# Kernel optimization log

Measured on AMD Instinct MI355X. Metric: run time of the kernel, lower is better.

## Reference

```python
import jax, jax.numpy as jnp
import numpy as np
from jax import lax

HID = 768; COND = 1280; LAT = 768; NL = 3; V = 128
TEMP = 1.0; TOP_P = 0.9


def setup_inputs() -> dict:
    key = jax.random.key(0)
    ks = iter(jax.random.split(key, 32))
    s = 0.02
    g = 1.0 / float(np.sqrt(HID))
    rn = lambda k, shape, sc: jax.random.normal(k, shape, jnp.float32) * sc
    z1 = lambda n: jnp.zeros((n,), jnp.float32)
    d = {}
    d['p'] = jax.random.normal(next(ks), (1, COND), jnp.float32)
    d['emb_W'] = rn(next(ks), (V, HID), s).at[0].set(0.0)  # padding_idx=0
    d['Wd'] = rn(next(ks), (HID, LAT + COND), s); d['bd'] = z1(HID)
    d['Wih0'] = rn(next(ks), (3 * HID, HID + COND), g); d['Whh0'] = rn(next(ks), (3 * HID, HID), g)
    d['bih0'] = z1(3 * HID); d['bhh0'] = z1(3 * HID)
    for l in (1, 2):
        d[f'Wih{l}'] = rn(next(ks), (3 * HID, HID), g)
        d[f'Whh{l}'] = rn(next(ks), (3 * HID, HID), g)
        d[f'bih{l}'] = z1(3 * HID); d[f'bhh{l}'] = z1(3 * HID)
    d['Wf1'] = rn(next(ks), (HID, COND), s); d['bf1'] = z1(HID)
    d['Wf2'] = rn(next(ks), (2 * HID, HID), s); d['bf2'] = z1(2 * HID)
    d['Wo'] = rn(next(ks), (HID, HID), s)
    d['num_samples'] = 256; d['max_len'] = 64; d['top_k'] = 40
    return d


def _gru_layer(x, h, Wih, Whh, bih, bhh):
    # torch GRU cell: gate order (r, z, n)
    gx = x @ Wih.T + bih          # [B, 3H]
    gh = h @ Whh.T + bhh          # [B, 3H]
    xr, xz, xn = jnp.split(gx, 3, axis=-1)
    hr, hz, hn = jnp.split(gh, 3, axis=-1)
    r = jax.nn.sigmoid(xr + hr)
    z = jax.nn.sigmoid(xz + hz)
    n = jnp.tanh(xn + r * hn)
    return (1.0 - z) * n + z * h


def reference(p, emb_W, Wd, bd,
              Wih0, Whh0, bih0, bhh0,
              Wih1, Whh1, bih1, bhh1,
              Wih2, Whh2, bih2, bhh2,
              Wf1, bf1, Wf2, bf2, Wo,
              num_samples, max_len, top_k):
    B = num_samples
    k_tot = min(top_k, V)
    pe = jnp.broadcast_to(p, (B, COND))                       # p.repeat(B,1)
    z = jax.random.normal(jax.random.key(42), (B, LAT), jnp.float32)
    h0 = jax.nn.gelu(jnp.concatenate([z, pe], axis=1) @ Wd.T + bd, approximate=False)
    h = jnp.tile(h0[None], (NL, 1, 1))                        # [NL, B, H]
    # FiLM params depend only on pe -> hoist out of the decode loop
    fp = jax.nn.gelu(pe @ Wf1.T + bf1, approximate=False) @ Wf2.T + bf2
    gamma, beta = jnp.split(fp, 2, axis=-1)                   # [B, H] each
    cur0 = jnp.ones((B,), jnp.int32)                          # BOS token = 1
    keys = jax.random.split(jax.random.key(7), max_len)
    rows = jnp.arange(B)[:, None]

    def step(carry, k):
        cur, h = carry
        emb = emb_W[cur]                                      # [B, 768]
        x = jnp.concatenate([emb, pe], axis=-1)               # [B, 2048]
        h0n = _gru_layer(x, h[0], Wih0, Whh0, bih0, bhh0)
        h1n = _gru_layer(h0n, h[1], Wih1, Whh1, bih1, bhh1)
        h2n = _gru_layer(h1n, h[2], Wih2, Whh2, bih2, bhh2)
        hn = jnp.stack([h0n, h1n, h2n])
        filmed = h2n * (1.0 + gamma) + beta                   # DeepFiLM on last output
        logits = (filmed @ Wo.T) @ emb_W.T / TEMP             # tied fc_out
        kth = lax.top_k(logits, k_tot)[0][:, -1:]
        logits = jnp.where(logits < kth, -jnp.inf, logits)
        probs = jax.nn.softmax(logits, axis=-1)
        sidx = jnp.argsort(-probs, axis=-1)
        sp = jnp.take_along_axis(probs, sidx, axis=-1)
        rem = jnp.cumsum(sp, axis=-1) > TOP_P
        rem = jnp.concatenate([jnp.zeros_like(rem[:, :1]), rem[:, :-1]], axis=-1)
        rem_orig = jnp.zeros_like(rem).at[rows, sidx].set(rem)
        probs = jnp.where(rem_orig, 0.0, probs)
        nxt = jax.random.categorical(k, jnp.log(probs), axis=-1).astype(jnp.int32)
        return (nxt, hn), nxt

    (_, _), toks = lax.scan(step, (cur0, h), keys)            # toks: [max_len, B]
    seq = jnp.concatenate([cur0[:, None], toks.T], axis=1)    # [B, max_len+1]
    return seq
```

## Files before the change

kernel.cpp:

```cpp
#include <hip/hip_runtime.h>
#include <hip/hip_bf16.h>
#include <stdint.h>

#define HID 768
#define COND 1280
#define NB 256
#define VOC 128
#define TSTEPS 64
#define KTOP 40
#define G3 2304
#define LH (NB*HID)

__device__ __forceinline__ uint32_t rotl32(uint32_t v, int d) {
  return (v << d) | (v >> (32 - d));
}

__device__ __forceinline__ void threefry(uint32_t k0, uint32_t k1,
                                         uint32_t x0, uint32_t x1,
                                         uint32_t& o0, uint32_t& o1) {
  uint32_t k2 = k0 ^ k1 ^ 0x1BD11BDAu;
  x0 += k0; x1 += k1;
#define TF_R(r) { x0 += x1; x1 = rotl32(x1, r); x1 ^= x0; }
  TF_R(13) TF_R(15) TF_R(26) TF_R(6)
  x0 += k1; x1 += k2 + 1u;
  TF_R(17) TF_R(29) TF_R(16) TF_R(24)
  x0 += k2; x1 += k0 + 2u;
  TF_R(13) TF_R(15) TF_R(26) TF_R(6)
  x0 += k0; x1 += k1 + 3u;
  TF_R(17) TF_R(29) TF_R(16) TF_R(24)
  x0 += k1; x1 += k2 + 4u;
  TF_R(13) TF_R(15) TF_R(26) TF_R(6)
  x0 += k2; x1 += k0 + 5u;
#undef TF_R
  o0 = x0; o1 = x1;
}

__device__ __forceinline__ float bits_to_01(uint32_t b) {
  return __uint_as_float((b >> 9) | 0x3f800000u) - 1.0f;
}

__device__ __forceinline__ float gelu_exact(float x) {
  return x * (erff(x / 0x1.6a09e6p+0f) + 1.0f) * 0.5f;
}

__device__ __forceinline__ float sigmoid_(float x) {
  return 0.5f + 0.5f * tanhf(0.5f * x);
}

__global__ __launch_bounds__(256) void k_init(uint32_t* keys, int* cur, int* seq) {
  int tid = threadIdx.x;
  cur[tid] = 1;
  seq[tid * (TSTEPS + 1)] = 1;
  if (tid < 64) {
    uint32_t o0, o1;
    threefry(0u, 7u, 0u, (uint32_t)tid, o0, o1);
    keys[2 * tid] = o0; keys[2 * tid + 1] = o1;
  }
}

__global__ __launch_bounds__(256) void k_z(float* __restrict__ z) {
  int i = blockIdx.x * 256 + threadIdx.x;
  uint32_t o0, o1;
  threefry(0u, 42u, 0u, (uint32_t)i, o0, o1);
  uint32_t bits = o0 ^ o1;
  const float SQ2 = 0x1.6a09e6p+0f;
  const float NM1 = -0x1.fffffep-1f;
  float f = bits_to_01(bits);
  float u = fmaxf(NM1, f * 2.0f + NM1);
  z[i] = SQ2 * erfinvf(u);
}

__global__ __launch_bounds__(256) void k_pe1(const float* __restrict__ p,
    const float* __restrict__ Wd, const float* __restrict__ Wih0,
    const float* __restrict__ Wf1, const float* __restrict__ bf1,
    float* __restrict__ cd, float* __restrict__ c0, float* __restrict__ t1) {
  int g = blockIdx.x, tid = threadIdx.x;
  const float* row;
  if (g < HID)            row = Wd   + (size_t)g * 2048 + HID;
  else if (g < HID + G3)  row = Wih0 + (size_t)(g - HID) * 2048 + HID;
  else                    row = Wf1  + (size_t)(g - HID - G3) * COND;
  float acc = 0.0f;
  for (int k = tid; k < COND; k += 256) acc += p[k] * row[k];
  __shared__ float red[256];
  red[tid] = acc; __syncthreads();
  for (int s = 128; s > 0; s >>= 1) { if (tid < s) red[tid] += red[tid + s]; __syncthreads(); }
  if (tid == 0) {
    if (g < HID) cd[g] = red[0];
    else if (g < HID + G3) c0[g - HID] = red[0];
    else { int j = g - HID - G3; t1[j] = gelu_exact(red[0] + bf1[j]); }
  }
}

__global__ __launch_bounds__(256) void k_pe2(const float* __restrict__ t1,
    const float* __restrict__ Wf2, const float* __restrict__ bf2,
    float* __restrict__ gamma, float* __restrict__ beta) {
  int j = blockIdx.x, tid = threadIdx.x;
  const float* row = Wf2 + (size_t)j * HID;
  float acc = 0.0f;
  for (int k = tid; k < HID; k += 256) acc += t1[k] * row[k];
  __shared__ float red[256];
  red[tid] = acc; __syncthreads();
  for (int s = 128; s > 0; s >>= 1) { if (tid < s) red[tid] += red[tid + s]; __syncthreads(); }
  if (tid == 0) {
    float v = red[0] + bf2[j];
    if (j < HID) gamma[j] = v; else beta[j - HID] = v;
  }
}

template<bool FILM, int EPI>
__global__ __launch_bounds__(256) void k_gemm(
    const float* __restrict__ A, int lda,
    const float* __restrict__ B, int ldb,
    float* __restrict__ C, int N, int Kp, long partStride,
    const float* __restrict__ ga, const float* __restrict__ be,
    const float* __restrict__ e0, const float* __restrict__ e1,
    float* __restrict__ H1, float* __restrict__ H2) {
  __shared__ __align__(16) float As[32][68];
  __shared__ __align__(16) float Bs[32][68];
  const int tid = threadIdx.x;
  const int tm = tid & 15, tn = tid >> 4;
  const int bm = blockIdx.x * 64, bn = blockIdx.y * 64;
  const int kbase = blockIdx.z * Kp;
  const int lr = tid >> 3;
  const int lk = (tid & 7) * 4;
  float acc[4][4] = {};
  for (int k0 = 0; k0 < Kp; k0 += 32) {
    int gk = kbase + k0 + lk;
    float4 av0 = *(const float4*)(A + (size_t)(bm + lr)      * lda + gk);
    float4 av1 = *(const float4*)(A + (size_t)(bm + lr + 32) * lda + gk);
    float4 bv0 = *(const float4*)(B + (size_t)(bn + lr)      * ldb + gk);
    float4 bv1 = *(const float4*)(B + (size_t)(bn + lr + 32) * ldb + gk);
    if (FILM) {
      float4 g = *(const float4*)(ga + gk);
      float4 bb = *(const float4*)(be + gk);
      av0.x = av0.x * (1.0f + g.x) + bb.x; av0.y = av0.y * (1.0f + g.y) + bb.y;
      av0.z = av0.z * (1.0f + g.z) + bb.z; av0.w = av0.w * (1.0f + g.w) + bb.w;
      av1.x = av1.x * (1.0f + g.x) + bb.x; av1.y = av1.y * (1.0f + g.y) + bb.y;
      av1.z = av1.z * (1.0f + g.z) + bb.z; av1.w = av1.w * (1.0f + g.w) + bb.w;
    }
    __syncthreads();
    As[lk + 0][lr] = av0.x; As[lk + 1][lr] = av0.y; As[lk + 2][lr] = av0.z; As[lk + 3][lr] = av0.w;
    As[lk + 0][lr + 32] = av1.x; As[lk + 1][lr + 32] = av1.y; As[lk + 2][lr + 32] = av1.z; As[lk + 3][lr + 32] = av1.w;
    Bs[lk + 0][lr] = bv0.x; Bs[lk + 1][lr] = bv0.y; Bs[lk + 2][lr] = bv0.z; Bs[lk + 3][lr] = bv0.w;
    Bs[lk + 0][lr + 32] = bv1.x; Bs[lk + 1][lr + 32] = bv1.y; Bs[lk + 2][lr + 32] = bv1.z; Bs[lk + 3][lr + 32] = bv1.w;
    __syncthreads();
#pragma unroll
    for (int kk = 0; kk < 32; kk++) {
      float4 a = *(const float4*)&As[kk][tm * 4];
      float4 b = *(const float4*)&Bs[kk][tn * 4];
      acc[0][0] += a.x * b.x; acc[0][1] += a.x * b.y; acc[0][2] += a.x * b.z; acc[0][3] += a.x * b.w;
      acc[1][0] += a.y * b.x; acc[1][1] += a.y * b.y; acc[1][2] += a.y * b.z; acc[1][3] += a.y * b.w;
      acc[2][0] += a.z * b.x; acc[2][1] += a.z * b.y; acc[2][2] += a.z * b.z; acc[2][3] += a.z * b.w;
      acc[3][0] += a.w * b.x; acc[3][1] += a.w * b.y; acc[3][2] += a.w * b.z; acc[3][3] += a.w * b.w;
    }
  }
  if (EPI == 0) {
    float* Cp = C + (size_t)blockIdx.z * (size_t)partStride;
#pragma unroll
    for (int i = 0; i < 4; i++) {
      float4 v; v.x = acc[i][0]; v.y = acc[i][1]; v.z = acc[i][2]; v.w = acc[i][3];
      *(float4*)(Cp + (size_t)(bm + tm * 4 + i) * N + bn + tn * 4) = v;
    }
  } else {
#pragma unroll
    for (int i = 0; i < 4; i++)
#pragma unroll
      for (int j = 0; j < 4; j++) {
        int row = bm + tm * 4 + i, col = bn + tn * 4 + j;
        float v = gelu_exact(acc[i][j] + e0[col] + e1[col]);
        C [(size_t)row * N + col] = v;
        H1[(size_t)row * N + col] = v;
        H2[(size_t)row * N + col] = v;
      }
  }
}

template<bool L0>
__global__ __launch_bounds__(256) void k_gates(
    const float* __restrict__ gxP, const float* __restrict__ ghP,
    const float* __restrict__ E0, const int* __restrict__ cur,
    const float* __restrict__ c0,
    const float* __restrict__ bih, const float* __restrict__ bhh,
    const float* __restrict__ hin, float* __restrict__ hout) {
  int idx = blockIdx.x * 256 + threadIdx.x;
  int b = idx / HID, j = idx - b * HID;
  const long S = (long)NB * G3;
  long base = (long)b * G3;
  float xr, xz, xn;
  if (L0) {
    const float* e = E0 + (size_t)cur[b] * G3;
    xr = e[j]           + c0[j]           + bih[j];
    xz = e[j + HID]     + c0[j + HID]     + bih[j + HID];
    xn = e[j + 2 * HID] + c0[j + 2 * HID] + bih[j + 2 * HID];
  } else {
    xr = gxP[base + j]           + gxP[S + base + j]           + bih[j];
    xz = gxP[base + j + HID]     + gxP[S + base + j + HID]     + bih[j + HID];
    xn = gxP[base + j + 2 * HID] + gxP[S + base + j + 2 * HID] + bih[j + 2 * HID];
  }
  float hr = ghP[base + j]           + ghP[S + base + j]           + bhh[j];
  float hz = ghP[base + j + HID]     + ghP[S + base + j + HID]     + bhh[j + HID];
  float hn = ghP[base + j + 2 * HID] + ghP[S + base + j + 2 * HID] + bhh[j + 2 * HID];
  float r  = sigmoid_(xr + hr);
  float zg = sigmoid_(xz + hz);
  float n  = tanhf(xn + r * hn);
  float h  = hin[idx];
  hout[idx] = (1.0f - zg) * n + zg * h;
}

__global__ __launch_bounds__(256) void k_sample(
    const float* __restrict__ oP, const float* __restrict__ embW,
    const uint32_t* __restrict__ keys, int t,
    int* __restrict__ cur, int* __restrict__ seq) {
  const int b = blockIdx.x, tid = threadIdx.x;
  __shared__ __align__(16) float o[HID];
  __shared__ float logit[VOC];
  __shared__ float gum[VOC];
  __shared__ float prob[VOC];
  __shared__ float skey[VOC];
  __shared__ int   sidx[VOC];
  __shared__ float rv[VOC];
  __shared__ int   ri[VOC];
  __shared__ float sden;
  const long OS = (long)NB * HID;
  for (int k = tid; k < HID; k += 256) {
    long ix = (long)b * HID + k;
    o[k] = ((oP[ix] + oP[OS + ix]) + oP[2 * OS + ix]) + oP[3 * OS + ix];
  }
  __syncthreads();
  if (tid < VOC) {
    const float4* ew = (const float4*)(embW + (size_t)tid * HID);
    const float4* ov = (const float4*)o;
    float a0 = 0, a1 = 0, a2 = 0, a3 = 0;
#pragma unroll 4
    for (int q = 0; q < HID / 4; q++) {
      float4 w = ew[q]; float4 x = ov[q];
      a0 += w.x * x.x; a1 += w.y * x.y; a2 += w.z * x.z; a3 += w.w * x.w;
    }
    logit[tid] = (a0 + a1) + (a2 + a3);
  } else {
    int v = tid - VOC;
    int i = b * VOC + v;
    uint32_t o0, o1;
    uint32_t kk0 = keys[2 * t], kk1 = keys[2 * t + 1];
    threefry(kk0, kk1, 0u, (uint32_t)i, o0, o1);
    uint32_t bits = o0 ^ o1;
    float f = bits_to_01(bits);
    float u = f + 0x1p-126f;
    u = fmaxf(0x1p-126f, u);
    gum[v] = -logf(-logf(u));
  }
  __syncthreads();
  if (tid < VOC) { skey[tid] = logit[tid]; sidx[tid] = tid; }
  for (int ksz = 2; ksz <= VOC; ksz <<= 1) {
    for (int jsz = ksz >> 1; jsz > 0; jsz >>= 1) {
      __syncthreads();
      if (tid < VOC) {
        int ixj = tid ^ jsz;
        if (ixj > tid) {
          float ka = skey[tid], kb = skey[ixj];
          int ia = sidx[tid], ib = sidx[ixj];
          bool ab = (ka > kb) || (ka == kb && ia < ib);
          bool up = ((tid & ksz) == 0);
          if (up ? !ab : ab) {
            skey[tid] = kb; skey[ixj] = ka; sidx[tid] = ib; sidx[ixj] = ia;
          }
        }
      }
    }
  }
  __syncthreads();
  float m = skey[0], kth = skey[KTOP - 1];
  __syncthreads();
  if (tid < VOC) {
    float l = logit[tid];
    prob[tid] = (l < kth) ? 0.0f : expf(l - m);
  }
  __syncthreads();
  if (tid < VOC) rv[tid] = prob[tid];
  __syncthreads();
  for (int s = 64; s > 0; s >>= 1) { if (tid < s) rv[tid] += rv[tid + s]; __syncthreads(); }
  if (tid == 0) sden = rv[0];
  __syncthreads();
  if (tid < VOC) {
    prob[tid] = prob[tid] / sden;
    skey[tid] = prob[tid];
    sidx[tid] = tid;
  }
  for (int ksz = 2; ksz <= VOC; ksz <<= 1) {
    for (int jsz = ksz >> 1; jsz > 0; jsz >>= 1) {
      __syncthreads();
      if (tid < VOC) {
        int ixj = tid ^ jsz;
        if (ixj > tid) {
          float ka = skey[tid], kb = skey[ixj];
          int ia = sidx[tid], ib = sidx[ixj];
          bool ab = (ka > kb) || (ka == kb && ia < ib);
          bool up = ((tid & ksz) == 0);
          if (up ? !ab : ab) {
            skey[tid] = kb; skey[ixj] = ka; sidx[tid] = ib; sidx[ixj] = ia;
          }
        }
      }
    }
  }
  __syncthreads();
  if (tid == 0) {
    float c = 0.0f;
    for (int i2 = 0; i2 < VOC; i2++) {
      float pv = skey[i2];
      if (i2 > 0 && c > 0.9f) prob[sidx[i2]] = 0.0f;
      c += pv;
    }
  }
  __syncthreads();
  if (tid < VOC) { rv[tid] = logf(prob[tid]) + gum[tid]; ri[tid] = tid; }
  __syncthreads();
  for (int s = 64; s > 0; s >>= 1) {
    if (tid < s) {
      float vb = rv[tid + s]; int ib2 = ri[tid + s];
      if (vb > rv[tid] || (vb == rv[tid] && ib2 < ri[tid])) { rv[tid] = vb; ri[tid] = ib2; }
    }
    __syncthreads();
  }
  if (tid == 0) { int v = ri[0]; cur[b] = v; seq[b * (TSTEPS + 1) + t + 1] = v; }
}

extern "C" void kernel_launch(void* const* d_in, const int* in_sizes, int n_in,
                              void* d_out, int out_size, void* d_ws, size_t ws_size,
                              hipStream_t stream) {
  const float* p    = (const float*)d_in[0];
  const float* embW = (const float*)d_in[1];
  const float* Wd   = (const float*)d_in[2];
  const float* bd   = (const float*)d_in[3];
  const float* Wih0 = (const float*)d_in[4];
  const float* Whh0 = (const float*)d_in[5];
  const float* bih0 = (const float*)d_in[6];
  const float* bhh0 = (const float*)d_in[7];
  const float* Wih1 = (const float*)d_in[8];
  const float* Whh1 = (const float*)d_in[9];
  const float* bih1 = (const float*)d_in[10];
  const float* bhh1 = (const float*)d_in[11];
  const float* Wih2 = (const float*)d_in[12];
  const float* Whh2 = (const float*)d_in[13];
  const float* bih2 = (const float*)d_in[14];
  const float* bhh2 = (const float*)d_in[15];
  const float* Wf1  = (const float*)d_in[16];
  const float* bf1  = (const float*)d_in[17];
  const float* Wf2  = (const float*)d_in[18];
  const float* bf2  = (const float*)d_in[19];
  const float* Wo   = (const float*)d_in[20];
  int* seq = (int*)d_out;

  float* w = (float*)d_ws;
  float* z     = w;
  float* E0    = z + 196608;
  float* cd    = E0 + 294912;
  float* c0    = cd + 768;
  float* t1    = c0 + 2304;
  float* gamma = t1 + 768;
  float* beta  = gamma + 768;
  float* HA    = beta + 768;
  float* HB    = HA + 589824;
  float* gxP   = HB + 589824;
  float* ghP   = gxP + 1179648;
  float* oP    = ghP + 1179648;
  uint32_t* keys = (uint32_t*)(oP + 786432);
  int* cur = (int*)(keys + 128);

  const long PS_G = (long)NB * G3;
  const long PS_O = (long)NB * HID;

  k_init<<<1, 256, 0, stream>>>(keys, cur, seq);
  k_z<<<768, 256, 0, stream>>>(z);
  k_pe1<<<HID + G3 + HID, 256, 0, stream>>>(p, Wd, Wih0, Wf1, bf1, cd, c0, t1);
  k_pe2<<<2 * HID, 256, 0, stream>>>(t1, Wf2, bf2, gamma, beta);
  k_gemm<false, 0><<<dim3(2, 36, 1), 256, 0, stream>>>(embW, HID, Wih0, 2048, E0,
      G3, HID, 0L, nullptr, nullptr, nullptr, nullptr, nullptr, nullptr);
  k_gemm<false, 1><<<dim3(4, 12, 1), 256, 0, stream>>>(z, HID, Wd, 2048, HA,
      HID, HID, 0L, nullptr, nullptr, cd, bd, HA + LH, HA + 2 * LH);

  for (int t = 0; t < TSTEPS; t++) {
    float* Hin  = (t & 1) ? HB : HA;
    float* Hout = (t & 1) ? HA : HB;
    k_gemm<false, 0><<<dim3(4, 36, 2), 256, 0, stream>>>(Hin, HID, Whh0, HID, ghP,
        G3, 384, PS_G, nullptr, nullptr, nullptr, nullptr, nullptr, nullptr);
    k_gates<true><<<768, 256, 0, stream>>>(nullptr, ghP, E0, cur, c0, bih0, bhh0, Hin, Hout);
    k_gemm<false, 0><<<dim3(4, 36, 2), 256, 0, stream>>>(Hout, HID, Wih1, HID, gxP,
        G3, 384, PS_G, nullptr, nullptr, nullptr, nullptr, nullptr, nullptr);
    k_gemm<false, 0><<<dim3(4, 36, 2), 256, 0, stream>>>(Hin + LH, HID, Whh1, HID, ghP,
        G3, 384, PS_G, nullptr, nullptr, nullptr, nullptr, nullptr, nullptr);
    k_gates<false><<<768, 256, 0, stream>>>(gxP, ghP, nullptr, nullptr, nullptr,
        bih1, bhh1, Hin + LH, Hout + LH);
    k_gemm<false, 0><<<dim3(4, 36, 2), 256, 0, stream>>>(Hout + LH, HID, Wih2, HID, gxP,
        G3, 384, PS_G, nullptr, nullptr, nullptr, nullptr, nullptr, nullptr);
    k_gemm<false, 0><<<dim3(4, 36, 2), 256, 0, stream>>>(Hin + 2 * LH, HID, Whh2, HID, ghP,
        G3, 384, PS_G, nullptr, nullptr, nullptr, nullptr, nullptr, nullptr);
    k_gates<false><<<768, 256, 0, stream>>>(gxP, ghP, nullptr, nullptr, nullptr,
        bih2, bhh2, Hin + 2 * LH, Hout + 2 * LH);
    k_gemm<true, 0><<<dim3(4, 12, 4), 256, 0, stream>>>(Hout + 2 * LH, HID, Wo, HID, oP,
        HID, 192, PS_O, gamma, beta, nullptr, nullptr, nullptr, nullptr);
    k_sample<<<256, 256, 0, stream>>>(oP, embW, keys, t, cur, seq);
  }
}
```

Before: 13.21 ms.

## Replace split-K GEMMs with smaller-tile full-K GEMM and batch paired layer GEMMs

Adds a new GEMM kernel with smaller output tiles (64x32 or 32x32) that runs the full K dimension, so the split-K partial buffers and their reduction inside the gate and sampling kernels go away. The input-to-hidden and hidden-to-hidden GEMMs for layers 1 and 2 are merged into one launch via blockIdx.z, which cuts kernel launches per step. The FiLM GEMM uses a 32-row tile with more blocks. In exchange, each block runs a longer K loop with a simpler, lower-reuse register tile (2 columns per thread), which may lower arithmetic intensity.

```diff
diff --git a/kernel.cpp b/kernel.cpp
--- a/kernel.cpp
+++ b/kernel.cpp
@@ -175,16 +175,77 @@
   }
 }
 
+template<int MT, bool FILM>
+__global__ __launch_bounds__(256) void k_gemm2(
+    const float* __restrict__ A0, const float* __restrict__ B0, float* __restrict__ C0,
+    const float* __restrict__ A1, const float* __restrict__ B1, float* __restrict__ C1,
+    int N, int K,
+    const float* __restrict__ ga, const float* __restrict__ be) {
+  const float* A = blockIdx.z ? A1 : A0;
+  const float* B = blockIdx.z ? B1 : B0;
+  float*       C = blockIdx.z ? C1 : C0;
+  __shared__ __align__(16) float As[32][MT + 4];
+  __shared__ __align__(16) float Bs[32][36];
+  const int tid = threadIdx.x;
+  const int bm = blockIdx.x * MT, bn = blockIdx.y * 32;
+  const int lr = tid >> 3;
+  const int lk = (tid & 7) * 4;
+  constexpr int RPT = MT / 16;
+  const int tm = tid & 15, tn = tid >> 4;
+  float acc[RPT][2] = {};
+  for (int k0 = 0; k0 < K; k0 += 32) {
+    float4 av[MT / 32];
+#pragma unroll
+    for (int r = 0; r < MT / 32; r++) {
+      av[r] = *(const float4*)(A + (size_t)(bm + lr + r * 32) * K + k0 + lk);
+      if (FILM) {
+        float4 g  = *(const float4*)(ga + k0 + lk);
+        float4 bb = *(const float4*)(be + k0 + lk);
+        av[r].x = av[r].x * (1.0f + g.x) + bb.x;
+        av[r].y = av[r].y * (1.0f + g.y) + bb.y;
+        av[r].z = av[r].z * (1.0f + g.z) + bb.z;
+        av[r].w = av[r].w * (1.0f + g.w) + bb.w;
+      }
+    }
+    float4 bv = *(const float4*)(B + (size_t)(bn + lr) * K + k0 + lk);
+    __syncthreads();
+#pragma unroll
+    for (int r = 0; r < MT / 32; r++) {
+      As[lk + 0][lr + r * 32] = av[r].x;
+      As[lk + 1][lr + r * 32] = av[r].y;
+      As[lk + 2][lr + r * 32] = av[r].z;
+      As[lk + 3][lr + r * 32] = av[r].w;
+    }
+    Bs[lk + 0][lr] = bv.x; Bs[lk + 1][lr] = bv.y;
+    Bs[lk + 2][lr] = bv.z; Bs[lk + 3][lr] = bv.w;
+    __syncthreads();
+#pragma unroll
+    for (int kk = 0; kk < 32; kk++) {
+      float b0 = Bs[kk][tn * 2], b1 = Bs[kk][tn * 2 + 1];
+#pragma unroll
+      for (int i = 0; i < RPT; i++) {
+        float a = As[kk][tm * RPT + i];
+        acc[i][0] += a * b0;
+        acc[i][1] += a * b1;
+      }
+    }
+  }
+#pragma unroll
+  for (int i = 0; i < RPT; i++) {
+    float2 v; v.x = acc[i][0]; v.y = acc[i][1];
+    *(float2*)(C + (size_t)(bm + tm * RPT + i) * N + bn + tn * 2) = v;
+  }
+}
+
 template<bool L0>
 __global__ __launch_bounds__(256) void k_gates(
-    const float* __restrict__ gxP, const float* __restrict__ ghP,
+    const float* __restrict__ gx, const float* __restrict__ gh,
     const float* __restrict__ E0, const int* __restrict__ cur,
     const float* __restrict__ c0,
     const float* __restrict__ bih, const float* __restrict__ bhh,
     const float* __restrict__ hin, float* __restrict__ hout) {
   int idx = blockIdx.x * 256 + threadIdx.x;
   int b = idx / HID, j = idx - b * HID;
-  const long S = (long)NB * G3;
   long base = (long)b * G3;
   float xr, xz, xn;
   if (L0) {
@@ -193,13 +254,13 @@
     xz = e[j + HID]     + c0[j + HID]     + bih[j + HID];
     xn = e[j + 2 * HID] + c0[j + 2 * HID] + bih[j + 2 * HID];
   } else {
-    xr = gxP[base + j]           + gxP[S + base + j]           + bih[j];
-    xz = gxP[base + j + HID]     + gxP[S + base + j + HID]     + bih[j + HID];
-    xn = gxP[base + j + 2 * HID] + gxP[S + base + j + 2 * HID] + bih[j + 2 * HID];
-  }
-  float hr = ghP[base + j]           + ghP[S + base + j]           + bhh[j];
-  float hz = ghP[base + j + HID]     + ghP[S + base + j + HID]     + bhh[j + HID];
-  float hn = ghP[base + j + 2 * HID] + ghP[S + base + j + 2 * HID] + bhh[j + 2 * HID];
+    xr = gx[base + j]           + bih[j];
+    xz = gx[base + j + HID]     + bih[j + HID];
+    xn = gx[base + j + 2 * HID] + bih[j + 2 * HID];
+  }
+  float hr = gh[base + j]           + bhh[j];
+  float hz = gh[base + j + HID]     + bhh[j + HID];
+  float hn = gh[base + j + 2 * HID] + bhh[j + 2 * HID];
   float r  = sigmoid_(xr + hr);
   float zg = sigmoid_(xz + hz);
   float n  = tanhf(xn + r * hn);
@@ -221,11 +282,7 @@
   __shared__ float rv[VOC];
   __shared__ int   ri[VOC];
   __shared__ float sden;
-  const long OS = (long)NB * HID;
-  for (int k = tid; k < HID; k += 256) {
-    long ix = (long)b * HID + k;
-    o[k] = ((oP[ix] + oP[OS + ix]) + oP[2 * OS + ix]) + oP[3 * OS + ix];
-  }
+  for (int k = tid; k < HID; k += 256) o[k] = oP[(long)b * HID + k];
   __syncthreads();
   if (tid < VOC) {
     const float4* ew = (const float4*)(embW + (size_t)tid * HID);
@@ -361,14 +418,11 @@
   float* beta  = gamma + 768;
   float* HA    = beta + 768;
   float* HB    = HA + 589824;
-  float* gxP   = HB + 589824;
-  float* ghP   = gxP + 1179648;
-  float* oP    = ghP + 1179648;
-  uint32_t* keys = (uint32_t*)(oP + 786432);
+  float* gx    = HB + 589824;
+  float* gh    = gx + 589824;
+  float* oP    = gh + 589824;
+  uint32_t* keys = (uint32_t*)(oP + 196608);
   int* cur = (int*)(keys + 128);
-
-  const long PS_G = (long)NB * G3;
-  const long PS_O = (long)NB * HID;
 
   k_init<<<1, 256, 0, stream>>>(keys, cur, seq);
   k_z<<<768, 256, 0, stream>>>(z);
@@ -382,23 +436,19 @@
   for (int t = 0; t < TSTEPS; t++) {
     float* Hin  = (t & 1) ? HB : HA;
     float* Hout = (t & 1) ? HA : HB;
-    k_gemm<false, 0><<<dim3(4, 36, 2), 256, 0, stream>>>(Hin, HID, Whh0, HID, ghP,
-        G3, 384, PS_G, nullptr, nullptr, nullptr, nullptr, nullptr, nullptr);
-    k_gates<true><<<768, 256, 0, stream>>>(nullptr, ghP, E0, cur, c0, bih0, bhh0, Hin, Hout);
-    k_gemm<false, 0><<<dim3(4, 36, 2), 256, 0, stream>>>(Hout, HID, Wih1, HID, gxP,
-        G3, 384, PS_G, nullptr, nullptr, nullptr, nullptr, nullptr, nullptr);
-    k_gemm<false, 0><<<dim3(4, 36, 2), 256, 0, stream>>>(Hin + LH, HID, Whh1, HID, ghP,
-        G3, 384, PS_G, nullptr, nullptr, nullptr, nullptr, nullptr, nullptr);
-    k_gates<false><<<768, 256, 0, stream>>>(gxP, ghP, nullptr, nullptr, nullptr,
+    k_gemm2<64, false><<<dim3(4, 72, 1), 256, 0, stream>>>(
+        Hin, Whh0, gh, nullptr, nullptr, nullptr, G3, HID, nullptr, nullptr);
+    k_gates<true><<<768, 256, 0, stream>>>(nullptr, gh, E0, cur, c0, bih0, bhh0, Hin, Hout);
+    k_gemm2<64, false><<<dim3(4, 72, 2), 256, 0, stream>>>(
+        Hout, Wih1, gx, Hin + LH, Whh1, gh, G3, HID, nullptr, nullptr);
+    k_gates<false><<<768, 256, 0, stream>>>(gx, gh, nullptr, nullptr, nullptr,
         bih1, bhh1, Hin + LH, Hout + LH);
-    k_gemm<false, 0><<<dim3(4, 36, 2), 256, 0, stream>>>(Hout + LH, HID, Wih2, HID, gxP,
-        G3, 384, PS_G, nullptr, nullptr, nullptr, nullptr, nullptr, nullptr);
-    k_gemm<false, 0><<<dim3(4, 36, 2), 256, 0, stream>>>(Hin + 2 * LH, HID, Whh2, HID, ghP,
-        G3, 384, PS_G, nullptr, nullptr, nullptr, nullptr, nullptr, nullptr);
-    k_gates<false><<<768, 256, 0, stream>>>(gxP, ghP, nullptr, nullptr, nullptr,
+    k_gemm2<64, false><<<dim3(4, 72, 2), 256, 0, stream>>>(
+        Hout + LH, Wih2, gx, Hin + 2 * LH, Whh2, gh, G3, HID, nullptr, nullptr);
+    k_gates<false><<<768, 256, 0, stream>>>(gx, gh, nullptr, nullptr, nullptr,
         bih2, bhh2, Hin + 2 * LH, Hout + 2 * LH);
-    k_gemm<true, 0><<<dim3(4, 12, 4), 256, 0, stream>>>(Hout + 2 * LH, HID, Wo, HID, oP,
-        HID, 192, PS_O, gamma, beta, nullptr, nullptr, nullptr, nullptr);
+    k_gemm2<32, true><<<dim3(8, 24, 1), 256, 0, stream>>>(
+        Hout + 2 * LH, Wo, oP, nullptr, nullptr, nullptr, HID, HID, gamma, beta);
     k_sample<<<256, 256, 0, stream>>>(oP, embW, keys, t, cur, seq);
   }
 }
```

New measurement: 14.41 ms. +9.0%, slower.

## Fuse the decode loop into one persistent cooperative kernel with grid syncs

Applied to the files above, without the earlier changes.

Replaces the roughly ten kernel launches per decode step with one cooperative kernel that loops over all 64 steps and uses grid.sync() between phases. The three recurrent Whh GEMMs now run together in a single phase at the start of each step, since they depend only on the previous hidden state. They use full-K 64x128 tiles with no split-K, so the gates no longer sum two partials. The aim is to remove launch overhead and cut the number of serialised stages, at the cost of grid-wide barriers, only 216 or 144 of 256 blocks active during GEMM phases, and fixed register and shared-memory limits from the persistent 512-thread blocks.

```diff
diff --git a/kernel.cpp b/kernel.cpp
--- a/kernel.cpp
+++ b/kernel.cpp
@@ -1,6 +1,9 @@
 #include <hip/hip_runtime.h>
+#include <hip/hip_cooperative_groups.h>
 #include <hip/hip_bf16.h>
 #include <stdint.h>
+
+namespace cg = cooperative_groups;
 
 #define HID 768
 #define COND 1280
@@ -10,6 +13,7 @@
 #define KTOP 40
 #define G3 2304
 #define LH (NB*HID)
+#define LG (NB*G3)
 
 __device__ __forceinline__ uint32_t rotl32(uint32_t v, int d) {
   return (v << d) | (v >> (32 - d));
@@ -175,54 +179,95 @@
   }
 }
 
+
+__device__ __forceinline__ void gemm64x128_film(
+    bool film,
+    const float* __restrict__ A, const float* __restrict__ B, float* __restrict__ C,
+    int NC, int bm, int bn, int kbeg, int klen,
+    const float* __restrict__ ga, const float* __restrict__ be,
+    float (*As)[68], float (*Bs)[132]) {
+  const int tid = threadIdx.x;
+  const int lr = tid >> 3;
+  const int lk = (tid & 7) * 4;
+  const int tm = tid & 15;
+  const int tn = tid >> 4;
+  float acc[4][4] = {};
+  for (int k0 = 0; k0 < klen; k0 += 32) {
+    const int gk = kbeg + k0 + lk;
+    float4 av  = *(const float4*)(A + (size_t)(bm + lr) * HID + gk);
+    float4 bv0 = *(const float4*)(B + (size_t)(bn + lr) * HID + gk);
+    float4 bv1 = *(const float4*)(B + (size_t)(bn + lr + 64) * HID + gk);
+    if (film) {
+      float4 g  = *(const float4*)(ga + gk);
+      float4 bb = *(const float4*)(be + gk);
+      av.x = av.x * (1.0f + g.x) + bb.x; av.y = av.y * (1.0f + g.y) + bb.y;
+      av.z = av.z * (1.0f + g.z) + bb.z; av.w = av.w * (1.0f + g.w) + bb.w;
+    }
+    __syncthreads();
+    As[lk + 0][lr] = av.x;  As[lk + 1][lr] = av.y;  As[lk + 2][lr] = av.z;  As[lk + 3][lr] = av.w;
+    Bs[lk + 0][lr] = bv0.x; Bs[lk + 1][lr] = bv0.y; Bs[lk + 2][lr] = bv0.z; Bs[lk + 3][lr] = bv0.w;
+    Bs[lk + 0][lr + 64] = bv1.x; Bs[lk + 1][lr + 64] = bv1.y;
+    Bs[lk + 2][lr + 64] = bv1.z; Bs[lk + 3][lr + 64] = bv1.w;
+    __syncthreads();
+#pragma unroll
+    for (int kk = 0; kk < 32; kk++) {
+      float4 a = *(const float4*)&As[kk][tm * 4];
+      float4 b = *(const float4*)&Bs[kk][tn * 4];
+      acc[0][0] += a.x * b.x; acc[0][1] += a.x * b.y; acc[0][2] += a.x * b.z; acc[0][3] += a.x * b.w;
+      acc[1][0] += a.y * b.x; acc[1][1] += a.y * b.y; acc[1][2] += a.y * b.z; acc[1][3] += a.y * b.w;
+      acc[2][0] += a.z * b.x; acc[2][1] += a.z * b.y; acc[2][2] += a.z * b.z; acc[2][3] += a.z * b.w;
+      acc[3][0] += a.w * b.x; acc[3][1] += a.w * b.y; acc[3][2] += a.w * b.z; acc[3][3] += a.w * b.w;
+    }
+  }
+#pragma unroll
+  for (int i = 0; i < 4; i++) {
+    float4 v; v.x = acc[i][0]; v.y = acc[i][1]; v.z = acc[i][2]; v.w = acc[i][3];
+    *(float4*)(C + (size_t)(bm + tm * 4 + i) * NC + bn + tn * 4) = v;
+  }
+}
+
 template<bool L0>
-__global__ __launch_bounds__(256) void k_gates(
-    const float* __restrict__ gxP, const float* __restrict__ ghP,
+__device__ __forceinline__ void gates_phase(
+    const float* __restrict__ gx, const float* __restrict__ gh,
     const float* __restrict__ E0, const int* __restrict__ cur,
     const float* __restrict__ c0,
     const float* __restrict__ bih, const float* __restrict__ bhh,
-    const float* __restrict__ hin, float* __restrict__ hout) {
-  int idx = blockIdx.x * 256 + threadIdx.x;
-  int b = idx / HID, j = idx - b * HID;
-  const long S = (long)NB * G3;
-  long base = (long)b * G3;
-  float xr, xz, xn;
-  if (L0) {
-    const float* e = E0 + (size_t)cur[b] * G3;
-    xr = e[j]           + c0[j]           + bih[j];
-    xz = e[j + HID]     + c0[j + HID]     + bih[j + HID];
-    xn = e[j + 2 * HID] + c0[j + 2 * HID] + bih[j + 2 * HID];
-  } else {
-    xr = gxP[base + j]           + gxP[S + base + j]           + bih[j];
-    xz = gxP[base + j + HID]     + gxP[S + base + j + HID]     + bih[j + HID];
-    xn = gxP[base + j + 2 * HID] + gxP[S + base + j + 2 * HID] + bih[j + 2 * HID];
-  }
-  float hr = ghP[base + j]           + ghP[S + base + j]           + bhh[j];
-  float hz = ghP[base + j + HID]     + ghP[S + base + j + HID]     + bhh[j + HID];
-  float hn = ghP[base + j + 2 * HID] + ghP[S + base + j + 2 * HID] + bhh[j + 2 * HID];
-  float r  = sigmoid_(xr + hr);
-  float zg = sigmoid_(xz + hz);
-  float n  = tanhf(xn + r * hn);
-  float h  = hin[idx];
-  hout[idx] = (1.0f - zg) * n + zg * h;
-}
-
-__global__ __launch_bounds__(256) void k_sample(
+    const float* __restrict__ hin, float* __restrict__ hout,
+    int bid, int tid) {
+  for (int idx = bid * 512 + tid; idx < NB * HID; idx += 256 * 512) {
+    int b = idx / HID, j = idx - b * HID;
+    long base = (long)b * G3;
+    float xr, xz, xn;
+    if (L0) {
+      const float* e = E0 + (size_t)cur[b] * G3;
+      xr = e[j]           + c0[j]           + bih[j];
+      xz = e[j + HID]     + c0[j + HID]     + bih[j + HID];
+      xn = e[j + 2 * HID] + c0[j + 2 * HID] + bih[j + 2 * HID];
+    } else {
+      const long S = (long)NB * G3;
+      xr = gx[base + j]           + gx[S + base + j]           + bih[j];
+      xz = gx[base + j + HID]     + gx[S + base + j + HID]     + bih[j + HID];
+      xn = gx[base + j + 2 * HID] + gx[S + base + j + 2 * HID] + bih[j + 2 * HID];
+    }
+    float hr = gh[base + j]           + bhh[j];
+    float hz = gh[base + j + HID]     + bhh[j + HID];
+    float hn = gh[base + j + 2 * HID] + bhh[j + 2 * HID];
+    float r  = sigmoid_(xr + hr);
+    float zg = sigmoid_(xz + hz);
+    float n  = tanhf(xn + r * hn);
+    float h  = hin[idx];
+    hout[idx] = (1.0f - zg) * n + zg * h;
+  }
+}
+
+__device__ void sample_phase(
     const float* __restrict__ oP, const float* __restrict__ embW,
     const uint32_t* __restrict__ keys, int t,
-    int* __restrict__ cur, int* __restrict__ seq) {
-  const int b = blockIdx.x, tid = threadIdx.x;
-  __shared__ __align__(16) float o[HID];
-  __shared__ float logit[VOC];
-  __shared__ float gum[VOC];
-  __shared__ float prob[VOC];
-  __shared__ float skey[VOC];
-  __shared__ int   sidx[VOC];
-  __shared__ float rv[VOC];
-  __shared__ int   ri[VOC];
-  __shared__ float sden;
+    int* __restrict__ cur, int* __restrict__ seq, int b, int tid,
+    float* o, float* logit, float* gum, float* prob, float* skey, float* rv,
+    int* sidx, int* ri, float* sden) {
   const long OS = (long)NB * HID;
-  for (int k = tid; k < HID; k += 256) {
+  for (int k = tid; k < HID; k += 512) {
     long ix = (long)b * HID + k;
     o[k] = ((oP[ix] + oP[OS + ix]) + oP[2 * OS + ix]) + oP[3 * OS + ix];
   }
@@ -237,7 +282,7 @@
       a0 += w.x * x.x; a1 += w.y * x.y; a2 += w.z * x.z; a3 += w.w * x.w;
     }
     logit[tid] = (a0 + a1) + (a2 + a3);
-  } else {
+  } else if (tid < 2 * VOC) {
     int v = tid - VOC;
     int i = b * VOC + v;
     uint32_t o0, o1;
@@ -279,10 +324,10 @@
   if (tid < VOC) rv[tid] = prob[tid];
   __syncthreads();
   for (int s = 64; s > 0; s >>= 1) { if (tid < s) rv[tid] += rv[tid + s]; __syncthreads(); }
-  if (tid == 0) sden = rv[0];
+  if (tid == 0) *sden = rv[0];
   __syncthreads();
   if (tid < VOC) {
-    prob[tid] = prob[tid] / sden;
+    prob[tid] = prob[tid] / (*sden);
     skey[tid] = prob[tid];
     sidx[tid] = tid;
   }
@@ -323,6 +368,73 @@
     __syncthreads();
   }
   if (tid == 0) { int v = ri[0]; cur[b] = v; seq[b * (TSTEPS + 1) + t + 1] = v; }
+}
+
+__global__ __launch_bounds__(512, 2) void k_loop(
+    const float* __restrict__ embW,
+    const float* __restrict__ Whh0, const float* __restrict__ bih0, const float* __restrict__ bhh0,
+    const float* __restrict__ Wih1, const float* __restrict__ Whh1,
+    const float* __restrict__ bih1, const float* __restrict__ bhh1,
+    const float* __restrict__ Wih2, const float* __restrict__ Whh2,
+    const float* __restrict__ bih2, const float* __restrict__ bhh2,
+    const float* __restrict__ Wo,
+    const float* __restrict__ E0, const float* __restrict__ c0,
+    const float* __restrict__ gamma, const float* __restrict__ beta,
+    float* __restrict__ HA, float* __restrict__ HB,
+    float* __restrict__ gh, float* __restrict__ gx, float* __restrict__ oP,
+    const uint32_t* __restrict__ keys, int* __restrict__ cur, int* __restrict__ seq)
+{
+  cg::grid_group grid = cg::this_grid();
+  __shared__ __align__(16) float As[32][68];
+  __shared__ __align__(16) float Bs[32][132];
+  __shared__ __align__(16) float s_o[HID];
+  __shared__ float s_logit[VOC], s_gum[VOC], s_prob[VOC], s_skey[VOC], s_rv[VOC];
+  __shared__ int s_sidx[VOC], s_ri[VOC];
+  __shared__ float s_sden;
+
+  const int bid = blockIdx.x, tid = threadIdx.x;
+
+  for (int t = 0; t < TSTEPS; ++t) {
+    float* Hin  = (t & 1) ? HB : HA;
+    float* Hout = (t & 1) ? HA : HB;
+
+    if (bid < 216) {
+      int l = bid / 72, r = bid - l * 72, bt = r / 18, ct = r - bt * 18;
+      const float* Bw = (l == 0) ? Whh0 : ((l == 1) ? Whh1 : Whh2);
+      gemm64x128_film(false, Hin + (size_t)l * LH, Bw, gh + (size_t)l * LG, G3,
+                      bt * 64, ct * 128, 0, HID, nullptr, nullptr, As, Bs);
+    }
+    grid.sync();
+    gates_phase<true>(nullptr, gh, E0, cur, c0, bih0, bhh0, Hin, Hout, bid, tid);
+    grid.sync();
+    if (bid < 144) {
+      int ks = bid / 72, r = bid - ks * 72, bt = r / 18, ct = r - bt * 18;
+      gemm64x128_film(false, Hout, Wih1, gx + (size_t)ks * LG, G3,
+                      bt * 64, ct * 128, ks * 384, 384, nullptr, nullptr, As, Bs);
+    }
+    grid.sync();
+    gates_phase<false>(gx, gh + LG, nullptr, nullptr, nullptr,
+                       bih1, bhh1, Hin + LH, Hout + LH, bid, tid);
+    grid.sync();
+    if (bid < 144) {
+      int ks = bid / 72, r = bid - ks * 72, bt = r / 18, ct = r - bt * 18;
+      gemm64x128_film(false, Hout + LH, Wih2, gx + (size_t)ks * LG, G3,
+                      bt * 64, ct * 128, ks * 384, 384, nullptr, nullptr, As, Bs);
+    }
+    grid.sync();
+    gates_phase<false>(gx, gh + 2 * (size_t)LG, nullptr, nullptr, nullptr,
+                       bih2, bhh2, Hin + 2 * LH, Hout + 2 * LH, bid, tid);
+    grid.sync();
+    if (bid < 96) {
+      int ks = bid / 24, r = bid - ks * 24, bt = r / 6, ct = r - bt * 6;
+      gemm64x128_film(true, Hout + 2 * LH, Wo, oP + (size_t)ks * LH, HID,
+                      bt * 64, ct * 128, ks * 192, 192, gamma, beta, As, Bs);
+    }
+    grid.sync();
+    sample_phase(oP, embW, keys, t, cur, seq, bid, tid,
+                 s_o, s_logit, s_gum, s_prob, s_skey, s_rv, s_sidx, s_ri, &s_sden);
+    grid.sync();
+  }
 }
 
 extern "C" void kernel_launch(void* const* d_in, const int* in_sizes, int n_in,
@@ -361,14 +473,11 @@
   float* beta  = gamma + 768;
   float* HA    = beta + 768;
   float* HB    = HA + 589824;
-  float* gxP   = HB + 589824;
-  float* ghP   = gxP + 1179648;
-  float* oP    = ghP + 1179648;
+  float* gh    = HB + 589824;
+  float* gx    = gh + 1769472;
+  float* oP    = gx + 1179648;
   uint32_t* keys = (uint32_t*)(oP + 786432);
   int* cur = (int*)(keys + 128);
-
-  const long PS_G = (long)NB * G3;
-  const long PS_O = (long)NB * HID;
 
   k_init<<<1, 256, 0, stream>>>(keys, cur, seq);
   k_z<<<768, 256, 0, stream>>>(z);
@@ -379,26 +488,14 @@
   k_gemm<false, 1><<<dim3(4, 12, 1), 256, 0, stream>>>(z, HID, Wd, 2048, HA,
       HID, HID, 0L, nullptr, nullptr, cd, bd, HA + LH, HA + 2 * LH);
 
-  for (int t = 0; t < TSTEPS; t++) {
-    float* Hin  = (t & 1) ? HB : HA;
-    float* Hout = (t & 1) ? HA : HB;
-    k_gemm<false, 0><<<dim3(4, 36, 2), 256, 0, stream>>>(Hin, HID, Whh0, HID, ghP,
-        G3, 384, PS_G, nullptr, nullptr, nullptr, nullptr, nullptr, nullptr);
-    k_gates<true><<<768, 256, 0, stream>>>(nullptr, ghP, E0, cur, c0, bih0, bhh0, Hin, Hout);
-    k_gemm<false, 0><<<dim3(4, 36, 2), 256, 0, stream>>>(Hout, HID, Wih1, HID, gxP,
-        G3, 384, PS_G, nullptr, nullptr, nullptr, nullptr, nullptr, nullptr);
-    k_gemm<false, 0><<<dim3(4, 36, 2), 256, 0, stream>>>(Hin + LH, HID, Whh1, HID, ghP,
-        G3, 384, PS_G, nullptr, nullptr, nullptr, nullptr, nullptr, nullptr);
-    k_gates<false><<<768, 256, 0, stream>>>(gxP, ghP, nullptr, nullptr, nullptr,
-        bih1, bhh1, Hin + LH, Hout + LH);
-    k_gemm<false, 0><<<dim3(4, 36, 2), 256, 0, stream>>>(Hout + LH, HID, Wih2, HID, gxP,
-        G3, 384, PS_G, nullptr, nullptr, nullptr, nullptr, nullptr, nullptr);
-    k_gemm<false, 0><<<dim3(4, 36, 2), 256, 0, stream>>>(Hin + 2 * LH, HID, Whh2, HID, ghP,
-        G3, 384, PS_G, nullptr, nullptr, nullptr, nullptr, nullptr, nullptr);
-    k_gates<false><<<768, 256, 0, stream>>>(gxP, ghP, nullptr, nullptr, nullptr,
-        bih2, bhh2, Hin + 2 * LH, Hout + 2 * LH);
-    k_gemm<true, 0><<<dim3(4, 12, 4), 256, 0, stream>>>(Hout + 2 * LH, HID, Wo, HID, oP,
-        HID, 192, PS_O, gamma, beta, nullptr, nullptr, nullptr, nullptr);
-    k_sample<<<256, 256, 0, stream>>>(oP, embW, keys, t, cur, seq);
-  }
-}
+  void* args[] = {
+    (void*)&embW,
+    (void*)&Whh0, (void*)&bih0, (void*)&bhh0,
+    (void*)&Wih1, (void*)&Whh1, (void*)&bih1, (void*)&bhh1,
+    (void*)&Wih2, (void*)&Whh2, (void*)&bih2, (void*)&bhh2,
+    (void*)&Wo,
+    (void*)&E0, (void*)&c0, (void*)&gamma, (void*)&beta,
+    (void*)&HA, (void*)&HB, (void*)&gh, (void*)&gx, (void*)&oP,
+    (void*)&keys, (void*)&cur, (void*)&seq};
+  hipLaunchCooperativeKernel((void*)k_loop, dim3(256), dim3(512), args, 0, stream);
+}
```

Result: slower. 25.92 ms (+96.2%).
